# Kernel tuning notes

Hardware: AMD Instinct MI355X
Metric: run time of the kernel (lower is better)

The kernel has to match this reference:

```python
import jax, jax.numpy as jnp
import numpy as np

T, N, H = 512, 256, 256
HR, WC = 64, 128   # mdp rows (== n_actions), mdp cols
V = 64             # size of 'values' observation


def setup_inputs() -> dict:
    key = jax.random.key(0)
    ks = jax.random.split(key, 20)
    def p(i, shape):
        return (jax.random.normal(ks[i], shape, jnp.float32) / np.sqrt(shape[0])).astype(jnp.float32)
    z = lambda *s: jnp.zeros(s, jnp.float32)
    return dict(
        values=jax.random.normal(ks[0], (T, N, V), jnp.float32),
        mdp=jax.random.normal(ks[1], (N, HR, WC), jnp.float32),
        actions=jax.random.randint(ks[2], (T, N), 0, HR),
        a0=jax.random.randint(ks[3], (N,), 0, HR),
        h0=jax.random.normal(ks[4], (N, H), jnp.float32) * 0.1,
        emb_W=p(5, (WC, H)), emb_b=z(H),
        gfw_Wih=p(6, (H, 3 * H)), gfw_Whh=p(7, (H, 3 * H)), gfw_bih=z(3 * H), gfw_bhh=z(3 * H),
        gbw_Wih=p(8, (H, 3 * H)), gbw_Whh=p(9, (H, 3 * H)), gbw_bih=z(3 * H), gbw_bhh=z(3 * H),
        f0_W=p(10, (V + H, H)), f0_b=z(H),
        f1_W=p(11, (H, H)), f1_b=z(H),
        cell_Wih=p(12, (H, 3 * H)), cell_Whh=p(13, (H, 3 * H)), cell_bih=z(3 * H), cell_bhh=z(3 * H),
        critic_W=p(14, (H, 1)), critic_b=z(1),
        qg_W=p(15, (H, 2 * H)), qg_b=z(2 * H),
    )


def gru_step(x, h, Wih, Whh, bih, bhh):
    # torch GRU gate math: gates ordered (reset, update, new)
    gi = x @ Wih + bih
    gh = h @ Whh + bhh
    ir, iz, in_ = jnp.split(gi, 3, axis=-1)
    hr, hz, hn = jnp.split(gh, 3, axis=-1)
    r = jax.nn.sigmoid(ir + hr)
    z = jax.nn.sigmoid(iz + hz)
    n = jnp.tanh(in_ + r * hn)
    return (1.0 - z) * n + z * h


def run_gru(seq, Wih, Whh, bih, bhh):
    # seq: (S, N, H) -> outputs (S, N, H), zero initial state (torch default)
    h0g = jnp.zeros((seq.shape[1], Whh.shape[0]), seq.dtype)
    def step(h, x):
        hn = gru_step(x, h, Wih, Whh, bih, bhh)
        return hn, hn
    _, out = jax.lax.scan(step, h0g, seq)
    return out


def _forward(values, mdp, actions, a0, h0,
             emb_W, emb_b,
             gfw_Wih, gfw_Whh, gfw_bih, gfw_bhh,
             gbw_Wih, gbw_Whh, gbw_bih, gbw_bhh,
             f0_W, f0_b, f1_W, f1_b,
             cell_Wih, cell_Whh, cell_bih, cell_bhh,
             critic_W, critic_b, qg_W, qg_b):
    M = mdp @ emb_W + emb_b                      # (N, HR, H) line embeddings
    seq = jnp.swapaxes(M, 0, 1)                  # (HR, N, H) seq-first
    Kf = run_gru(seq, gfw_Wih, gfw_Whh, gfw_bih, gfw_bhh)
    Kb = run_gru(seq[::-1], gbw_Wih, gbw_Whh, gbw_bih, gbw_bhh)[::-1]
    K = jnp.swapaxes(jnp.concatenate([Kf, Kb], -1), 0, 1)   # (N, HR, 2H)

    a_prev = jnp.concatenate([a0[None], actions[:-1]], axis=0)  # A[t-1], t=0 wraps to hx.a
    batch = jnp.arange(M.shape[0])

    def step(h, xs):
        v_t, ap, ac = xs
        r = M[batch, ap]                         # one-hot(a_prev) @ M == row gather, (N, H)
        x = jnp.concatenate([v_t, r], axis=-1)
        x = jax.nn.relu(x @ f0_W + f0_b)
        x = jax.nn.relu(x @ f1_W + f1_b)
        h = gru_step(x, h, cell_Wih, cell_Whh, cell_bih, cell_bhh)
        k = h @ qg_W + qg_b                      # (N, 2H) query
        logits = jnp.einsum('nsd,nd->ns', K, k)  # (N, HR)
        probs = jax.nn.softmax(logits, axis=-1)
        v = h @ critic_W + critic_b              # (N, 1)
        return h, (ac.astype(jnp.float32)[:, None], v, h, probs)

    _, (a_out, v_out, h_out, p_out) = jax.lax.scan(step, h0, (values, a_prev, actions))
    # pack() order: RecurrentState fields 'a v h a_probs'
    hx = jnp.concatenate([a_out, v_out, h_out, p_out], axis=-1)  # (T, N, 2+H+HR)
    return hx


def reference(values, mdp, actions, a0, h0,
              emb_W, emb_b,
              gfw_Wih, gfw_Whh, gfw_bih, gfw_bhh,
              gbw_Wih, gbw_Whh, gbw_bih, gbw_bhh,
              f0_W, f0_b, f1_W, f1_b,
              cell_Wih, cell_Whh, cell_bih, cell_bhh,
              critic_W, critic_b, qg_W, qg_b):
    return _forward(values, mdp, actions, a0, h0,
                    emb_W, emb_b,
                    gfw_Wih, gfw_Whh, gfw_bih, gfw_bhh,
                    gbw_Wih, gbw_Whh, gbw_bih, gbw_bhh,
                    f0_W, f0_b, f1_W, f1_b,
                    cell_Wih, cell_Whh, cell_bih, cell_bhh,
                    critic_W, critic_b, qg_W, qg_b)
```

## Files before the change

kernel.cpp:

```cpp
#include <hip/hip_runtime.h>

#define TSTEPS 512
#define NBATCH 256
#define HID    256
#define TCHUNK 64
#define NCHUNK 8

typedef __attribute__((ext_vector_type(8))) short bf16x8;
typedef __attribute__((ext_vector_type(4))) float f32x4;

__device__ __forceinline__ unsigned short f2b(float x) {
    union { float f; unsigned int u; } c; c.f = x;
    unsigned int u = c.u;
    return (unsigned short)((u + 0x7fffu + ((u >> 16) & 1u)) >> 16);
}

__device__ __forceinline__ void gload_lds16(const float* g, float* l) {
    __builtin_amdgcn_global_load_lds(
        (const __attribute__((address_space(1))) unsigned int*)g,
        (__attribute__((address_space(3))) unsigned int*)l,
        16, 0, 0);
}

__device__ __forceinline__ int swzi(int row, int g) {
// ... 76 lines not shown
                C[(long)row * ldc + col] = v;
            }
        }
}

__global__ void combine_bias(const float* a0, const float* b0,
                             const float* a1, const float* b1,
                             const float* a2, const float* b2,
                             float* o0, float* o1, float* o2)
{
    int i = blockIdx.x * 256 + threadIdx.x;
    o0[i] = a0[i] + b0[i];
    o1[i] = a1[i] + b1[i];
    o2[i] = a2[i] + b2[i];
}

__global__ void seq_major(const float* __restrict__ M, float* __restrict__ Mseq)
{
    int b = blockIdx.x;
    int s = b >> 8, n = b & 255;
    int t = threadIdx.x;
    Mseq[(long)b * 256 + t] = M[((long)n * 64 + s) * 256 + t];
}

__global__ __launch_bounds__(256) void pack_w(
    const float* __restrict__ Wf, const float* __restrict__ Wb, const float* __restrict__ Wc,
    unsigned short* __restrict__ Pf, unsigned short* __restrict__ Pb, unsigned short* __restrict__ Pc)
{
    int chunk = blockIdx.x * 256 + threadIdx.x;
    const float* W = (blockIdx.y == 0) ? Wf : ((blockIdx.y == 1) ? Wb : Wc);
    unsigned short* P = (blockIdx.y == 0) ? Pf : ((blockIdx.y == 1) ? Pb : Pc);
    int lane = chunk & 63;
    int kt   = (chunk >> 6) & 7;
    int f    = (chunk >> 9) % 6;
    int w    = chunk / 3072;
    int g = f >> 1, hh = f & 1;
    int c = lane & 15, q = lane >> 4;
    int col = g * 256 + w * 32 + hh * 16 + c;
    int k0  = kt * 32 + q * 8;
    unsigned int v[8];
#pragma unroll
    for (int j = 0; j < 8; j++) v[j] = f2b(W[(long)(k0 + j) * 768 + col]);
    uint4 o;
    o.x = v[0] | (v[1] << 16); o.y = v[2] | (v[3] << 16);
    o.z = v[4] | (v[5] << 16); o.w = v[6] | (v[7] << 16);
    *(uint4*)&P[(long)chunk * 8] = o;
}

__global__ void build_x(const float* __restrict__ values, const float* __restrict__ Mbuf,
                        const int* __restrict__ actions, const int* __restrict__ a0,
                        float* __restrict__ Xc, int t0)
{
    int m = blockIdx.x;
    int tl = m >> 8, n = m & 255;
    int t = t0 + tl;
    int c = threadIdx.x;
    float v;
    if (c < 64) {
        v = values[((long)t * 256 + n) * 64 + c];
    } else {
        int ap = (t == 0) ? a0[n] : actions[(long)(t - 1) * 256 + n];
        v = Mbuf[((long)n * 64 + ap) * 256 + (c - 64)];
    }
    Xc[(long)m * 320 + c] = v;
}

struct GemmRole {
    const float* A; const float* B; const float* bias; float* C;
    int K; long lda; long ldb; long ldc; int act; int nblocks; int ntn;
};

union FusedLds {
    struct { unsigned short hbuf[2][16][264]; float gibuf[2][16 * 772]; } s;
    struct { unsigned short As[64][32]; unsigned short Bs[128][32]; } g;
    struct { unsigned short As2[2][64][32]; unsigned short Bs2[2][64][32]; } l;
};

__device__ __forceinline__ void scan_role(FusedLds* L,
    const float* gi, const unsigned short* PK, const float* h_init,
    float* outp, float* h_state, int n0, int steps, int kgru, int d)
{
    auto& hbuf  = L->s.hbuf;
    auto& gibuf = L->s.gibuf;
    const int tid = threadIdx.x;
    const int w = tid >> 6, lane = tid & 63;
    const int q = lane >> 4, c = lane & 15, q8 = q << 3;
    const int wcol = w * 32;

    bf16x8 Bf[6][8];
#pragma unroll
    for (int f = 0; f < 6; f++)
#pragma unroll
        for (int kt = 0; kt < 8; kt++)
            Bf[f][kt] = *(const bf16x8*)&PK[(((long)(w * 6 + f) * 8 + kt) * 64 + lane) * 8];

    f32x4 hreg[2];
#pragma unroll
    for (int hh = 0; hh < 2; hh++)
#pragma unroll
        for (int rg = 0; rg < 4; rg++) {
            float v = 0.f;
            if (!kgru) v = h_init[(long)(n0 + q * 4 + rg) * 256 + wcol + hh * 16 + c];
            hreg[hh][rg] = v;
            hbuf[1][q * 4 + rg][wcol + hh * 16 + c] = f2b(v);
        }

    const int row0 = kgru ? (d ? 63 : 0) : 0;
    const long gstride = (kgru && d) ? -196608L : 196608L;
    const float* gsrc = gi + ((long)row0 * 256 + n0) * 768;
    float* optr[4];
    long ostride;
    if (kgru) {
        ostride = d ? -512L : 512L;
#pragma unroll
        for (int rg = 0; rg < 4; rg++)
            optr[rg] = outp + ((long)(n0 + q * 4 + rg) * 64 + row0) * 512 + d * 256 + wcol + c;
    } else {
        ostride = 65536L;
#pragma unroll
        for (int rg = 0; rg < 4; rg++)
            optr[rg] = outp + (long)(n0 + q * 4 + rg) * 256 + wcol + c;
    }

#pragma unroll
    for (int i = 0; i < 6; i++) {
        int idx = w * 6 + i;
        int r = idx / 3, ch = idx % 3;
        gload_lds16(gsrc + (long)r * 768 + ch * 256 + lane * 4,
                    &gibuf[0][r * 772 + ch * 256]);
    }
    __syncthreads();

    for (int s = 0; s < steps; s++) {
        const int cur = s & 1;
        if (s + 1 < steps) {
            const float* src = gsrc + gstride;
#pragma unroll
            for (int i = 0; i < 6; i++) {
                int idx = w * 6 + i;
                int r = idx / 3, ch = idx % 3;
                gload_lds16(src + (long)r * 768 + ch * 256 + lane * 4,
                            &gibuf[cur ^ 1][r * 772 + ch * 256]);
            }
        }
        gsrc += gstride;
        asm volatile("" ::: "memory");

        const unsigned short* hrd = &hbuf[cur ^ 1][0][0];
        const float* gp = &gibuf[cur][(q * 4) * 772 + wcol + c];
        unsigned short* hwr = &hbuf[cur][q * 4][wcol + c];

#pragma unroll
        for (int hh = 0; hh < 2; hh++) {
            f32x4 ar = (f32x4){0.f, 0.f, 0.f, 0.f};
            f32x4 az = (f32x4){0.f, 0.f, 0.f, 0.f};
            f32x4 an = (f32x4){0.f, 0.f, 0.f, 0.f};
#pragma unroll
            for (int kt = 0; kt < 8; kt++) {
                bf16x8 a = *(const bf16x8*)&hrd[c * 264 + kt * 32 + q8];
                ar = __builtin_amdgcn_mfma_f32_16x16x32_bf16(a, Bf[0 + hh][kt], ar, 0, 0, 0);
                az = __builtin_amdgcn_mfma_f32_16x16x32_bf16(a, Bf[2 + hh][kt], az, 0, 0, 0);
                an = __builtin_amdgcn_mfma_f32_16x16x32_bf16(a, Bf[4 + hh][kt], an, 0, 0, 0);
            }
#pragma unroll
            for (int rg = 0; rg < 4; rg++) {
                float gr = gp[rg * 772 +       hh * 16];
                float gz = gp[rg * 772 + 256 + hh * 16];
                float gn = gp[rg * 772 + 512 + hh * 16];
                float r  = __builtin_amdgcn_rcpf(1.f + __expf(-(gr + ar[rg])));
                float zg = __builtin_amdgcn_rcpf(1.f + __expf(-(gz + az[rg])));
                float nn = 1.f - 2.f * __builtin_amdgcn_rcpf(1.f + __expf(2.f * (gn + r * an[rg])));
                float hv = (1.f - zg) * nn + zg * hreg[hh][rg];
                hreg[hh][rg] = hv;
                hwr[rg * 264 + hh * 16] = f2b(hv);
                optr[rg][hh * 16] = hv;
            }
            asm volatile("" ::: "memory");
        }

#pragma unroll
        for (int rg = 0; rg < 4; rg++) optr[rg] += ostride;

        asm volatile("s_waitcnt vmcnt(8) lgkmcnt(0)" ::: "memory");
        __builtin_amdgcn_sched_barrier(0);
        __builtin_amdgcn_s_barrier();
        __builtin_amdgcn_sched_barrier(0);
    }

    if (!kgru) {
#pragma unroll
        for (int hh = 0; hh < 2; hh++)
#pragma unroll
            for (int rg = 0; rg < 4; rg++)
                h_state[(long)(n0 + q * 4 + rg) * 256 + wcol + hh * 16 + c] = hreg[hh][rg];
    }
}

__device__ __forceinline__ void gemm_role(FusedLds* L, const GemmRole& R, int rb)
{
    auto& As = L->g.As;
    auto& Bs = L->g.Bs;
    const int tid = threadIdx.x;
    const int lane = tid & 63, w = tid >> 6;
    const int mt = rb / R.ntn, nt = rb % R.ntn;
    const long m0 = (long)mt * 64, n0 = (long)nt * 128;
    const int wr = (w >> 2) * 32, wc = (w & 3) * 32;

    f32x4 acc[2][2];
#pragma unroll
    for (int i = 0; i < 2; i++)
#pragma unroll
        for (int j = 0; j < 2; j++) acc[i][j] = (f32x4){0.f, 0.f, 0.f, 0.f};

    for (int k0 = 0; k0 < R.K; k0 += 32) {
        {
            const int r = tid >> 3, ck = (tid & 7) << 2;
            const float* s = R.A + (m0 + r) * R.lda + k0 + ck;
            float4 v = *(const float4*)s;
            unsigned short* dp = &As[r][swzi(r, ck >> 3) + (ck & 7)];
            dp[0] = f2b(v.x); dp[1] = f2b(v.y); dp[2] = f2b(v.z); dp[3] = f2b(v.w);
        }
        {
            const int kk = tid >> 4, cn = (tid & 15) << 3;
            const float* s = R.B + (long)(k0 + kk) * R.ldb + n0 + cn;
            float4 v0 = *(const float4*)s, v1 = *(const float4*)(s + 4);
            const int sc = swzi(cn, kk >> 3) + (kk & 7);
            Bs[cn + 0][sc] = f2b(v0.x); Bs[cn + 1][sc] = f2b(v0.y);
            Bs[cn + 2][sc] = f2b(v0.z); Bs[cn + 3][sc] = f2b(v0.w);
            Bs[cn + 4][sc] = f2b(v1.x); Bs[cn + 5][sc] = f2b(v1.y);
            Bs[cn + 6][sc] = f2b(v1.z); Bs[cn + 7][sc] = f2b(v1.w);
        }
        __syncthreads();
        const int l15 = lane & 15, q = lane >> 4;
        bf16x8 a0 = *(const bf16x8*)&As[wr +      l15][swzi(wr +      l15, q)];
        bf16x8 a1 = *(const bf16x8*)&As[wr + 16 + l15][swzi(wr + 16 + l15, q)];
        bf16x8 b0 = *(const bf16x8*)&Bs[wc +      l15][swzi(wc +      l15, q)];
        bf16x8 b1 = *(const bf16x8*)&Bs[wc + 16 + l15][swzi(wc + 16 + l15, q)];
        acc[0][0] = __builtin_amdgcn_mfma_f32_16x16x32_bf16(a0, b0, acc[0][0], 0, 0, 0);
        acc[0][1] = __builtin_amdgcn_mfma_f32_16x16x32_bf16(a0, b1, acc[0][1], 0, 0, 0);
        acc[1][0] = __builtin_amdgcn_mfma_f32_16x16x32_bf16(a1, b0, acc[1][0], 0, 0, 0);
        acc[1][1] = __builtin_amdgcn_mfma_f32_16x16x32_bf16(a1, b1, acc[1][1], 0, 0, 0);
        __syncthreads();
    }
    const int cq = lane >> 4, cc = lane & 15;
#pragma unroll
    for (int i = 0; i < 2; i++)
#pragma unroll
        for (int j = 0; j < 2; j++) {
#pragma unroll
            for (int rg = 0; rg < 4; rg++) {
                long row = m0 + wr + i * 16 + cq * 4 + rg;
                long col = n0 + wc + j * 16 + cc;
                float v = acc[i][j][rg];
                if (R.bias) v += R.bias[col];
                if (R.act == 1) v = v > 0.f ? v : 0.f;
                R.C[row * R.ldc + col] = v;
            }
        }
}

__device__ __forceinline__ void logits_role(FusedLds* L, int rb,
    const float* Qs, const float* Kb, float* Lout)
{
    auto& As = L->l.As2;
    auto& Bs = L->l.Bs2;
    const int tid = threadIdx.x;
    const int half = tid >> 8, htid = tid & 255;
    const int z = rb * 2 + half;
    const float* A = Qs + (long)z * 512;
    const float* B = Kb + (long)z * 32768;
    float* C = Lout + (long)z * 64;
    const int lane = htid & 63, w4 = htid >> 6;
    const int wr = (w4 >> 1) * 32, wc = (w4 & 1) * 32;

    f32x4 acc[2][2];
#pragma unroll
    for (int i = 0; i < 2; i++)
#pragma unroll
        for (int j = 0; j < 2; j++) acc[i][j] = (f32x4){0.f, 0.f, 0.f, 0.f};

    for (int k0 = 0; k0 < 512; k0 += 32) {
        const int r = htid >> 2, ck = (htid & 3) << 3;
        {
            const float* s = A + (long)r * 131072 + k0 + ck;
            float4 v0 = *(const float4*)s, v1 = *(const float4*)(s + 4);
            unsigned short* d = &As[half][r][swzi(r, ck >> 3)];
            d[0] = f2b(v0.x); d[1] = f2b(v0.y); d[2] = f2b(v0.z); d[3] = f2b(v0.w);
            d[4] = f2b(v1.x); d[5] = f2b(v1.y); d[6] = f2b(v1.z); d[7] = f2b(v1.w);
        }
        {
            const float* s = B + (long)r * 512 + k0 + ck;
            float4 v0 = *(const float4*)s, v1 = *(const float4*)(s + 4);
            unsigned short* d = &Bs[half][r][swzi(r, ck >> 3)];
            d[0] = f2b(v0.x); d[1] = f2b(v0.y); d[2] = f2b(v0.z); d[3] = f2b(v0.w);
            d[4] = f2b(v1.x); d[5] = f2b(v1.y); d[6] = f2b(v1.z); d[7] = f2b(v1.w);
        }
        __syncthreads();
        const int l15 = lane & 15, q = lane >> 4;
        bf16x8 a0 = *(const bf16x8*)&As[half][wr +      l15][swzi(wr +      l15, q)];
        bf16x8 a1 = *(const bf16x8*)&As[half][wr + 16 + l15][swzi(wr + 16 + l15, q)];
        bf16x8 b0 = *(const bf16x8*)&Bs[half][wc +      l15][swzi(wc +      l15, q)];
        bf16x8 b1 = *(const bf16x8*)&Bs[half][wc + 16 + l15][swzi(wc + 16 + l15, q)];
        acc[0][0] = __builtin_amdgcn_mfma_f32_16x16x32_bf16(a0, b0, acc[0][0], 0, 0, 0);
        acc[0][1] = __builtin_amdgcn_mfma_f32_16x16x32_bf16(a0, b1, acc[0][1], 0, 0, 0);
        acc[1][0] = __builtin_amdgcn_mfma_f32_16x16x32_bf16(a1, b0, acc[1][0], 0, 0, 0);
        acc[1][1] = __builtin_amdgcn_mfma_f32_16x16x32_bf16(a1, b1, acc[1][1], 0, 0, 0);
        __syncthreads();
    }
    const int cq = lane >> 4, cc = lane & 15;
#pragma unroll
    for (int i = 0; i < 2; i++)
#pragma unroll
        for (int j = 0; j < 2; j++) {
#pragma unroll
            for (int rg = 0; rg < 4; rg++)
                C[(long)(wr + i * 16 + cq * 4 + rg) * 16384 + wc + j * 16 + cc] = acc[i][j][rg];
        }
}

__device__ __forceinline__ void epi_role(int rb,
    const float* Hall, const float* Lc, const int* actions,
    const float* critic_W, const float* critic_b, float* out, int t0)
{
    const int w = threadIdx.x >> 6, j = threadIdx.x & 63;
    const int m = rb * 8 + w;
    const int tl = m >> 8, n = m & 255;
    const int t = t0 + tl;
    long o = ((long)t * 256 + n) * 322;
    const float* h = Hall + (long)m * 256;
    float part = 0.f;
#pragma unroll
    for (int i = 0; i < 4; i++) {
        float hv = h[j + 64 * i];
        out[o + 2 + j + 64 * i] = hv;
        part += hv * critic_W[j + 64 * i];
    }
    for (int off = 32; off > 0; off >>= 1) part += __shfl_down(part, off);
    if (j == 0) {
        out[o]     = (float)actions[(long)t * 256 + n];
        out[o + 1] = part + critic_b[0];
    }
    float x = Lc[(long)m * 64 + j];
    float mx = x;
    for (int off = 32; off > 0; off >>= 1) mx = fmaxf(mx, __shfl_down(mx, off));
    mx = __shfl(mx, 0);
    float e = __expf(x - mx);
    float ssum = e;
    for (int off = 32; off > 0; off >>= 1) ssum += __shfl_down(ssum, off);
    ssum = __shfl(ssum, 0);
    out[o + 258 + j] = e / ssum;
}

__device__ __forceinline__ void bx_role(int rb,
    const float* values, const float* Mbuf, const int* actions, const int* a0,
    float* Xd, int t0)
{
    const int tid = threadIdx.x;
    if (tid >= 320) return;
    for (int rr = 0; rr < 128; rr++) {
        int m = rb * 128 + rr;
        int tl = m >> 8, n = m & 255;
        int t = t0 + tl;
        float v;
        if (tid < 64) {
            v = values[((long)t * 256 + n) * 64 + tid];
        } else {
            int ap = (t == 0) ? a0[n] : actions[(long)(t - 1) * 256 + n];
            v = Mbuf[((long)n * 64 + ap) * 256 + (tid - 64)];
        }
        Xd[(long)m * 320 + tid] = v;
    }
}

__global__ __launch_bounds__(512, 2) void fused_k(
    const float* sc_gi, const unsigned short* sc_PK, const float* sc_hinit,
    float* sc_out, float* sc_hstate,
    int kgru_nblk, const float* kg_gi0, const float* kg_gi1,
    const unsigned short* kg_PK0, const unsigned short* kg_PK1, float* kg_out,
    GemmRole g0, GemmRole g1, GemmRole g2, GemmRole g3,
    int lg_nblk, const float* lg_Q, const float* lg_K, float* lg_L,
    int ep_nblk, const float* ep_Hall, const float* ep_L, int ep_t0,
    int bx_nblk, const float* values, const float* Mbuf,
    const int* actions, const int* a0, float* bx_dst, int bx_t0,
    const float* critic_W, const float* critic_b, float* out)
{
    __shared__ __align__(16) FusedLds L;
    int b = blockIdx.x;
    if (b < 16) {
        scan_role(&L, sc_gi, sc_PK, sc_hinit, sc_out, sc_hstate, b * 16, TCHUNK, 0, 0);
        return;
    }
    b -= 16;
    if (b < kgru_nblk) {
        int d = b >> 4, n0 = (b & 15) * 16;
        scan_role(&L, d ? kg_gi1 : kg_gi0, d ? kg_PK1 : kg_PK0, nullptr,
                  kg_out, nullptr, n0, 64, 1, d);
        return;
    }
    b -= kgru_nblk;
    if (b < g0.nblocks) { gemm_role(&L, g0, b); return; }
    b -= g0.nblocks;
    if (b < g1.nblocks) { gemm_role(&L, g1, b); return; }
    b -= g1.nblocks;
    if (b < g2.nblocks) { gemm_role(&L, g2, b); return; }
    b -= g2.nblocks;
    if (b < g3.nblocks) { gemm_role(&L, g3, b); return; }
    b -= g3.nblocks;
    if (b < lg_nblk) { logits_role(&L, b, lg_Q, lg_K, lg_L); return; }
    b -= lg_nblk;
    if (b < ep_nblk) { epi_role(b, ep_Hall, ep_L, actions, critic_W, critic_b, out, ep_t0); return; }
    b -= ep_nblk;
    if (b < bx_nblk) bx_role(b, values, Mbuf, actions, a0, bx_dst, bx_t0);
}

__global__ __launch_bounds__(64) void epilogue_k(
    const float* __restrict__ Hallc, const float* __restrict__ Lc,
    const int* __restrict__ actions,
    const float* __restrict__ critic_W, const float* __restrict__ critic_b,
    float* __restrict__ out, int t0)
{
    int m = blockIdx.x;
    int tl = m >> 8, n = m & 255;
    int t = t0 + tl;
    int j = threadIdx.x;
    long o = ((long)t * 256 + n) * 322;
    const float* h = Hallc + (long)m * 256;
    float part = 0.f;
#pragma unroll
    for (int i = 0; i < 4; i++) {
        float hv = h[j + 64 * i];
        out[o + 2 + j + 64 * i] = hv;
        part += hv * critic_W[j + 64 * i];
    }
    for (int off = 32; off > 0; off >>= 1) part += __shfl_down(part, off);
    if (j == 0) {
        out[o]     = (float)actions[(long)t * 256 + n];
        out[o + 1] = part + critic_b[0];
    }
    float x = Lc[(long)m * 64 + j];
    float mx = x;
    for (int off = 32; off > 0; off >>= 1) mx = fmaxf(mx, __shfl_down(mx, off));
    mx = __shfl(mx, 0);
    float e = __expf(x - mx);
    float ssum = e;
    for (int off = 32; off > 0; off >>= 1) ssum += __shfl_down(ssum, off);
// ... 27 lines not shown
    const float* cell_Wih = (const float*)d_in[19];
    const float* cell_Whh = (const float*)d_in[20];
    const float* cell_bih = (const float*)d_in[21];
    const float* cell_bhh = (const float*)d_in[22];
    const float* critic_W = (const float*)d_in[23];
    const float* critic_b = (const float*)d_in[24];
    const float* qg_W     = (const float*)d_in[25];
    const float* qg_b     = (const float*)d_in[26];
    float* out = (float*)d_out;

    char* base = (char*)d_ws;
    size_t off = 0;
    auto alloc = [&](size_t nf) -> float* {
        float* p = (float*)(base + off);
        off += nf * sizeof(float);
        off = (off + 255) & ~(size_t)255;
        return p;
    };
    float* Mbuf   = alloc(16384ull * 256);
    float* Mseq   = alloc(16384ull * 256);
    float* gfA    = alloc(16384ull * 768);
    float* gbA    = alloc(16384ull * 768);
    float* Kbuf   = alloc(256ull * 64 * 512);
    float* PKf    = alloc(98304);
    float* PKb    = alloc(98304);
    float* PKc    = alloc(98304);
    float* hstate = alloc(256ull * 256);
    float* Xr[2]    = { alloc(16384ull * 320), alloc(16384ull * 320) };
    float* X0r[2]   = { alloc(16384ull * 256), alloc(16384ull * 256) };
    float* X1r[2]   = { alloc(16384ull * 256), alloc(16384ull * 256) };
    float* GIr[2]   = { alloc(16384ull * 768), alloc(16384ull * 768) };
    float* Hallr[4] = { alloc(16384ull * 256), alloc(16384ull * 256),
                        Mseq, alloc(16384ull * 256) };
    float* Qr[2]  = { gfA, gbA };
    float* Lr[2]  = { alloc(16384ull * 64), alloc(16384ull * 64) };
    float* bias_f = alloc(768);
    float* bias_b = alloc(768);
    float* bias_c = alloc(768);
    (void)ws_size; (void)in_sizes; (void)n_in; (void)out_size;

    dim3 blk(256);

    gemm_f32<false, 0><<<dim3(4, 256, 1), blk, 0, stream>>>(
        mdp, 128, 0, emb_W, 256, 0, emb_b, Mbuf, 256, 0, 16384, 256, 128);
    seq_major<<<dim3(16384), blk, 0, stream>>>(Mbuf, Mseq);
    pack_w<<<dim3(96, 3, 1), blk, 0, stream>>>(
        gfw_Whh, gbw_Whh, cell_Whh,
        (unsigned short*)PKf, (unsigned short*)PKb, (unsigned short*)PKc);
    combine_bias<<<dim3(3), blk, 0, stream>>>(gfw_bih, gfw_bhh, gbw_bih, gbw_bhh,
                                              cell_bih, cell_bhh, bias_f, bias_b, bias_c);
    gemm_f32<false, 0><<<dim3(12, 256, 1), blk, 0, stream>>>(
        Mseq, 256, 0, gfw_Wih, 768, 0, bias_f, gfA, 768, 0, 16384, 768, 256);
    gemm_f32<false, 0><<<dim3(12, 256, 1), blk, 0, stream>>>(
        Mseq, 256, 0, gbw_Wih, 768, 0, bias_b, gbA, 768, 0, 16384, 768, 256);

    build_x<<<dim3(16384), dim3(320), 0, stream>>>(values, Mbuf, actions, a0, Xr[0], 0);
    gemm_f32<false, 1><<<dim3(4, 256, 1), blk, 0, stream>>>(
        Xr[0], 320, 0, f0_W, 256, 0, f0_b, X0r[0], 256, 0, 16384, 256, 320);
    build_x<<<dim3(16384), dim3(320), 0, stream>>>(values, Mbuf, actions, a0, Xr[1], 64);
    gemm_f32<false, 1><<<dim3(4, 256, 1), blk, 0, stream>>>(
        Xr[1], 320, 0, f0_W, 256, 0, f0_b, X0r[1], 256, 0, 16384, 256, 320);
    gemm_f32<false, 1><<<dim3(4, 256, 1), blk, 0, stream>>>(
        X0r[0], 256, 0, f1_W, 256, 0, f1_b, X1r[0], 256, 0, 16384, 256, 256);
    build_x<<<dim3(16384), dim3(320), 0, stream>>>(values, Mbuf, actions, a0, Xr[0], 128);
    gemm_f32<false, 1><<<dim3(4, 256, 1), blk, 0, stream>>>(
        Xr[0], 320, 0, f0_W, 256, 0, f0_b, X0r[0], 256, 0, 16384, 256, 320);
    gemm_f32<false, 1><<<dim3(4, 256, 1), blk, 0, stream>>>(
        X0r[1], 256, 0, f1_W, 256, 0, f1_b, X1r[1], 256, 0, 16384, 256, 256);
    build_x<<<dim3(16384), dim3(320), 0, stream>>>(values, Mbuf, actions, a0, Xr[1], 192);
    gemm_f32<false, 0><<<dim3(12, 256, 1), blk, 0, stream>>>(
        X1r[0], 256, 0, cell_Wih, 768, 0, bias_c, GIr[0], 768, 0, 16384, 768, 256);

    for (int c = 0; c < NCHUNK; c++) {
        GemmRole g0{}, g1{}, g2{}, g3{};
        if (c <= 4) g0 = GemmRole{ Xr[(c + 1) & 1], f0_W, f0_b, X0r[(c + 1) & 1],
                                   320, 320, 256, 256, 1, 512, 2 };
        if (c <= 5) g1 = GemmRole{ X0r[c & 1], f1_W, f1_b, X1r[c & 1],
                                   256, 256, 256, 256, 1, 512, 2 };
        if (c <= 6) g2 = GemmRole{ X1r[(c + 1) & 1], cell_Wih, bias_c, GIr[(c + 1) & 1],
                                   256, 256, 768, 768, 0, 1536, 6 };
        if (c >= 1) g3 = GemmRole{ Hallr[(c - 1) & 3], qg_W, qg_b, Qr[(c - 1) & 1],
                                   256, 256, 512, 512, 0, 1024, 4 };
        int kgn = (c == 0) ? 32 : 0;
        int lgn = (c >= 2) ? 128 : 0;
        int epn = (c >= 3) ? 2048 : 0;
        int bxn = (c <= 3) ? 128 : 0;
        int total = 16 + kgn + g0.nblocks + g1.nblocks + g2.nblocks + g3.nblocks
                    + lgn + epn + bxn;

        fused_k<<<dim3(total), dim3(512), 0, stream>>>(
            GIr[c & 1], (const unsigned short*)PKc, (c == 0) ? h0 : (const float*)hstate,
            Hallr[c & 3], hstate,
            kgn, gfA, gbA, (const unsigned short*)PKf, (const unsigned short*)PKb, Kbuf,
            g0, g1, g2, g3,
            lgn, Qr[(c - 2) & 1], Kbuf, Lr[(c - 2) & 1],
            epn, Hallr[(c - 3) & 3], Lr[(c - 3) & 1], (c - 3) * 64,
            bxn, values, Mbuf, actions, a0, Xr[c & 1], (c + 4) * 64,
            critic_W, critic_b, out);
    }

    epilogue_k<<<dim3(16384), dim3(64), 0, stream>>>(
        Hallr[1], Lr[1], actions, critic_W, critic_b, out, 5 * 64);
    gemm_f32<false, 0><<<dim3(8, 256, 1), blk, 0, stream>>>(
        Hallr[3], 256, 0, qg_W, 512, 0, qg_b, Qr[1], 512, 0, 16384, 512, 256);
    gemm_f32<true, 0><<<dim3(1, 1, 256), blk, 0, stream>>>(
        Qr[0], 131072, 512, Kbuf, 512, 32768, nullptr, Lr[0], 16384, 64, 64, 64, 512);
    epilogue_k<<<dim3(16384), dim3(64), 0, stream>>>(
        Hallr[2], Lr[0], actions, critic_W, critic_b, out, 6 * 64);
    gemm_f32<true, 0><<<dim3(1, 1, 256), blk, 0, stream>>>(
        Qr[1], 131072, 512, Kbuf, 512, 32768, nullptr, Lr[1], 16384, 64, 64, 64, 512);
    epilogue_k<<<dim3(16384), dim3(64), 0, stream>>>(
        Hallr[3], Lr[1], actions, critic_W, critic_b, out, 7 * 64);
}
```

Before: 2.123 ms.

## Halve fused kernel block size to 256 threads with 4 waves per scan block

The fused persistent kernel moves from 512 to 256 threads per block. Each scan wave now owns 64 hidden columns with 12 B fragments held in registers, and the packed weight layout changes to match. The MFMA passes for the four column groups are interleaved with the gate math so tensor work overlaps the transcendental math, and the h tile is loaded into registers once per step. GEMM and logits roles are retiled to 64x64 tiles with twice as many blocks, and the build_x role is adjusted for 256 threads. The aim is cheaper barriers per sequential step on the latency-bound recurrence, at the cost of much higher register pressure (96 bf16x8 weight fragments per lane) and possible spilling.

Result: slower. 4.819 ms (+127.0%).

```diff
diff --git a/kernel.cpp b/kernel.cpp
--- a/kernel.cpp
+++ b/kernel.cpp
@@ -132,11 +132,11 @@
     unsigned short* P = (blockIdx.y == 0) ? Pf : ((blockIdx.y == 1) ? Pb : Pc);
     int lane = chunk & 63;
     int kt   = (chunk >> 6) & 7;
-    int f    = (chunk >> 9) % 6;
-    int w    = chunk / 3072;
-    int g = f >> 1, hh = f & 1;
+    int f    = (chunk >> 9) % 12;
+    int w    = chunk / 6144;
+    int g = f >> 2, hh = f & 3;
     int c = lane & 15, q = lane >> 4;
-    int col = g * 256 + w * 32 + hh * 16 + c;
+    int col = g * 256 + w * 64 + hh * 16 + c;
     int k0  = kt * 32 + q * 8;
     unsigned int v[8];
 #pragma unroll
@@ -172,9 +172,38 @@
 
 union FusedLds {
     struct { unsigned short hbuf[2][16][264]; float gibuf[2][16 * 772]; } s;
-    struct { unsigned short As[64][32]; unsigned short Bs[128][32]; } g;
-    struct { unsigned short As2[2][64][32]; unsigned short Bs2[2][64][32]; } l;
+    struct { unsigned short As[64][32]; unsigned short Bs[64][32]; } g;
 };
+
+#define MPASS(HH, PR, PZ, PN)                                                  \
+    do {                                                                       \
+        PR = (f32x4){0.f, 0.f, 0.f, 0.f};                                      \
+        PZ = (f32x4){0.f, 0.f, 0.f, 0.f};                                      \
+        PN = (f32x4){0.f, 0.f, 0.f, 0.f};                                      \
+        _Pragma("unroll")                                                      \
+        for (int kt = 0; kt < 8; kt++) {                                       \
+            PR = __builtin_amdgcn_mfma_f32_16x16x32_bf16(a[kt], Bf[0 + HH][kt], PR, 0, 0, 0); \
+            PZ = __builtin_amdgcn_mfma_f32_16x16x32_bf16(a[kt], Bf[4 + HH][kt], PZ, 0, 0, 0); \
+            PN = __builtin_amdgcn_mfma_f32_16x16x32_bf16(a[kt], Bf[8 + HH][kt], PN, 0, 0, 0); \
+        }                                                                      \
+    } while (0)
+
+#define GATES(HH, PR, PZ, PN)                                                  \
+    do {                                                                       \
+        _Pragma("unroll")                                                      \
+        for (int rg = 0; rg < 4; rg++) {                                       \
+            float gr = gp[rg * 772 +       HH * 16];                           \
+            float gz = gp[rg * 772 + 256 + HH * 16];                           \
+            float gn = gp[rg * 772 + 512 + HH * 16];                           \
+            float r  = __builtin_amdgcn_rcpf(1.f + __expf(-(gr + PR[rg])));    \
+            float zg = __builtin_amdgcn_rcpf(1.f + __expf(-(gz + PZ[rg])));    \
+            float nn = 1.f - 2.f * __builtin_amdgcn_rcpf(1.f + __expf(2.f * (gn + r * PN[rg]))); \
+            float hv = (1.f - zg) * nn + zg * hreg[HH][rg];                    \
+            hreg[HH][rg] = hv;                                                 \
+            hwr[rg * 264 + HH * 16] = f2b(hv);                                 \
+            optr[rg][HH * 16] = hv;                                            \
+        }                                                                      \
+    } while (0)
 
 __device__ __forceinline__ void scan_role(FusedLds* L,
     const float* gi, const unsigned short* PK, const float* h_init,
@@ -185,18 +214,18 @@
     const int tid = threadIdx.x;
     const int w = tid >> 6, lane = tid & 63;
     const int q = lane >> 4, c = lane & 15, q8 = q << 3;
-    const int wcol = w * 32;
-
-    bf16x8 Bf[6][8];
-#pragma unroll
-    for (int f = 0; f < 6; f++)
+    const int wcol = w * 64;
+
+    bf16x8 Bf[12][8];
+#pragma unroll
+    for (int f = 0; f < 12; f++)
 #pragma unroll
         for (int kt = 0; kt < 8; kt++)
-            Bf[f][kt] = *(const bf16x8*)&PK[(((long)(w * 6 + f) * 8 + kt) * 64 + lane) * 8];
-
-    f32x4 hreg[2];
-#pragma unroll
-    for (int hh = 0; hh < 2; hh++)
+            Bf[f][kt] = *(const bf16x8*)&PK[(((long)(w * 12 + f) * 8 + kt) * 64 + lane) * 8];
+
+    f32x4 hreg[4];
+#pragma unroll
+    for (int hh = 0; hh < 4; hh++)
 #pragma unroll
         for (int rg = 0; rg < 4; rg++) {
             float v = 0.f;
@@ -223,8 +252,8 @@
     }
 
 #pragma unroll
-    for (int i = 0; i < 6; i++) {
-        int idx = w * 6 + i;
+    for (int i = 0; i < 12; i++) {
+        int idx = w * 12 + i;
         int r = idx / 3, ch = idx % 3;
         gload_lds16(gsrc + (long)r * 768 + ch * 256 + lane * 4,
                     &gibuf[0][r * 772 + ch * 256]);
@@ -233,11 +262,12 @@
 
     for (int s = 0; s < steps; s++) {
         const int cur = s & 1;
+
         if (s + 1 < steps) {
             const float* src = gsrc + gstride;
 #pragma unroll
-            for (int i = 0; i < 6; i++) {
-                int idx = w * 6 + i;
+            for (int i = 0; i < 12; i++) {
+                int idx = w * 12 + i;
                 int r = idx / 3, ch = idx % 3;
                 gload_lds16(src + (long)r * 768 + ch * 256 + lane * 4,
                             &gibuf[cur ^ 1][r * 772 + ch * 256]);
@@ -250,38 +280,25 @@
         const float* gp = &gibuf[cur][(q * 4) * 772 + wcol + c];
         unsigned short* hwr = &hbuf[cur][q * 4][wcol + c];
 
-#pragma unroll
-        for (int hh = 0; hh < 2; hh++) {
-            f32x4 ar = (f32x4){0.f, 0.f, 0.f, 0.f};
-            f32x4 az = (f32x4){0.f, 0.f, 0.f, 0.f};
-            f32x4 an = (f32x4){0.f, 0.f, 0.f, 0.f};
-#pragma unroll
-            for (int kt = 0; kt < 8; kt++) {
-                bf16x8 a = *(const bf16x8*)&hrd[c * 264 + kt * 32 + q8];
-                ar = __builtin_amdgcn_mfma_f32_16x16x32_bf16(a, Bf[0 + hh][kt], ar, 0, 0, 0);
-                az = __builtin_amdgcn_mfma_f32_16x16x32_bf16(a, Bf[2 + hh][kt], az, 0, 0, 0);
-                an = __builtin_amdgcn_mfma_f32_16x16x32_bf16(a, Bf[4 + hh][kt], an, 0, 0, 0);
-            }
-#pragma unroll
-            for (int rg = 0; rg < 4; rg++) {
-                float gr = gp[rg * 772 +       hh * 16];
-                float gz = gp[rg * 772 + 256 + hh * 16];
-                float gn = gp[rg * 772 + 512 + hh * 16];
-                float r  = __builtin_amdgcn_rcpf(1.f + __expf(-(gr + ar[rg])));
-                float zg = __builtin_amdgcn_rcpf(1.f + __expf(-(gz + az[rg])));
-                float nn = 1.f - 2.f * __builtin_amdgcn_rcpf(1.f + __expf(2.f * (gn + r * an[rg])));
-                float hv = (1.f - zg) * nn + zg * hreg[hh][rg];
-                hreg[hh][rg] = hv;
-                hwr[rg * 264 + hh * 16] = f2b(hv);
-                optr[rg][hh * 16] = hv;
-            }
-            asm volatile("" ::: "memory");
-        }
+        bf16x8 a[8];
+#pragma unroll
+        for (int kt = 0; kt < 8; kt++)
+            a[kt] = *(const bf16x8*)&hrd[c * 264 + kt * 32 + q8];
+
+        f32x4 p0r, p0z, p0n, p1r, p1z, p1n;
+        MPASS(0, p0r, p0z, p0n);
+        MPASS(1, p1r, p1z, p1n);
+        GATES(0, p0r, p0z, p0n);
+        MPASS(2, p0r, p0z, p0n);
+        GATES(1, p1r, p1z, p1n);
+        MPASS(3, p1r, p1z, p1n);
+        GATES(2, p0r, p0z, p0n);
+        GATES(3, p1r, p1z, p1n);
 
 #pragma unroll
         for (int rg = 0; rg < 4; rg++) optr[rg] += ostride;
 
-        asm volatile("s_waitcnt vmcnt(8) lgkmcnt(0)" ::: "memory");
+        asm volatile("s_waitcnt vmcnt(16) lgkmcnt(0)" ::: "memory");
         __builtin_amdgcn_sched_barrier(0);
         __builtin_amdgcn_s_barrier();
         __builtin_amdgcn_sched_barrier(0);
@@ -289,7 +306,7 @@
 
     if (!kgru) {
 #pragma unroll
-        for (int hh = 0; hh < 2; hh++)
+        for (int hh = 0; hh < 4; hh++)
 #pragma unroll
             for (int rg = 0; rg < 4; rg++)
                 h_state[(long)(n0 + q * 4 + rg) * 256 + wcol + hh * 16 + c] = hreg[hh][rg];
@@ -303,8 +320,8 @@
     const int tid = threadIdx.x;
     const int lane = tid & 63, w = tid >> 6;
     const int mt = rb / R.ntn, nt = rb % R.ntn;
-    const long m0 = (long)mt * 64, n0 = (long)nt * 128;
-    const int wr = (w >> 2) * 32, wc = (w & 3) * 32;
+    const long m0 = (long)mt * 64, n0 = (long)nt * 64;
+    const int wr = (w >> 1) * 32, wc = (w & 1) * 32;
 
     f32x4 acc[2][2];
 #pragma unroll
@@ -314,14 +331,15 @@
 
     for (int k0 = 0; k0 < R.K; k0 += 32) {
         {
-            const int r = tid >> 3, ck = (tid & 7) << 2;
+            const int r = tid >> 2, ck = (tid & 3) << 3;
             const float* s = R.A + (m0 + r) * R.lda + k0 + ck;
-            float4 v = *(const float4*)s;
-            unsigned short* dp = &As[r][swzi(r, ck >> 3) + (ck & 7)];
-            dp[0] = f2b(v.x); dp[1] = f2b(v.y); dp[2] = f2b(v.z); dp[3] = f2b(v.w);
+            float4 v0 = *(const float4*)s, v1 = *(const float4*)(s + 4);
+            unsigned short* d = &As[r][swzi(r, ck >> 3)];
+            d[0] = f2b(v0.x); d[1] = f2b(v0.y); d[2] = f2b(v0.z); d[3] = f2b(v0.w);
+            d[4] = f2b(v1.x); d[5] = f2b(v1.y); d[6] = f2b(v1.z); d[7] = f2b(v1.w);
         }
         {
-            const int kk = tid >> 4, cn = (tid & 15) << 3;
+            const int kk = tid >> 3, cn = (tid & 7) << 3;
             const float* s = R.B + (long)(k0 + kk) * R.ldb + n0 + cn;
             float4 v0 = *(const float4*)s, v1 = *(const float4*)(s + 4);
             const int sc = swzi(cn, kk >> 3) + (kk & 7);
@@ -362,16 +380,15 @@
 __device__ __forceinline__ void logits_role(FusedLds* L, int rb,
     const float* Qs, const float* Kb, float* Lout)
 {
-    auto& As = L->l.As2;
-    auto& Bs = L->l.Bs2;
+    auto& As = L->g.As;
+    auto& Bs = L->g.Bs;
     const int tid = threadIdx.x;
-    const int half = tid >> 8, htid = tid & 255;
-    const int z = rb * 2 + half;
+    const int z = rb;
     const float* A = Qs + (long)z * 512;
     const float* B = Kb + (long)z * 32768;
     float* C = Lout + (long)z * 64;
-    const int lane = htid & 63, w4 = htid >> 6;
-    const int wr = (w4 >> 1) * 32, wc = (w4 & 1) * 32;
+    const int lane = tid & 63, w = tid >> 6;
+    const int wr = (w >> 1) * 32, wc = (w & 1) * 32;
 
     f32x4 acc[2][2];
 #pragma unroll
@@ -380,27 +397,27 @@
         for (int j = 0; j < 2; j++) acc[i][j] = (f32x4){0.f, 0.f, 0.f, 0.f};
 
     for (int k0 = 0; k0 < 512; k0 += 32) {
-        const int r = htid >> 2, ck = (htid & 3) << 3;
+        const int r = tid >> 2, ck = (tid & 3) << 3;
         {
             const float* s = A + (long)r * 131072 + k0 + ck;
             float4 v0 = *(const float4*)s, v1 = *(const float4*)(s + 4);
-            unsigned short* d = &As[half][r][swzi(r, ck >> 3)];
+            unsigned short* d = &As[r][swzi(r, ck >> 3)];
             d[0] = f2b(v0.x); d[1] = f2b(v0.y); d[2] = f2b(v0.z); d[3] = f2b(v0.w);
             d[4] = f2b(v1.x); d[5] = f2b(v1.y); d[6] = f2b(v1.z); d[7] = f2b(v1.w);
         }
         {
             const float* s = B + (long)r * 512 + k0 + ck;
             float4 v0 = *(const float4*)s, v1 = *(const float4*)(s + 4);
-            unsigned short* d = &Bs[half][r][swzi(r, ck >> 3)];
+            unsigned short* d = &Bs[r][swzi(r, ck >> 3)];
             d[0] = f2b(v0.x); d[1] = f2b(v0.y); d[2] = f2b(v0.z); d[3] = f2b(v0.w);
             d[4] = f2b(v1.x); d[5] = f2b(v1.y); d[6] = f2b(v1.z); d[7] = f2b(v1.w);
         }
         __syncthreads();
         const int l15 = lane & 15, q = lane >> 4;
-        bf16x8 a0 = *(const bf16x8*)&As[half][wr +      l15][swzi(wr +      l15, q)];
-        bf16x8 a1 = *(const bf16x8*)&As[half][wr + 16 + l15][swzi(wr + 16 + l15, q)];
-        bf16x8 b0 = *(const bf16x8*)&Bs[half][wc +      l15][swzi(wc +      l15, q)];
-        bf16x8 b1 = *(const bf16x8*)&Bs[half][wc + 16 + l15][swzi(wc + 16 + l15, q)];
+        bf16x8 a0 = *(const bf16x8*)&As[wr +      l15][swzi(wr +      l15, q)];
+        bf16x8 a1 = *(const bf16x8*)&As[wr + 16 + l15][swzi(wr + 16 + l15, q)];
+        bf16x8 b0 = *(const bf16x8*)&Bs[wc +      l15][swzi(wc +      l15, q)];
+        bf16x8 b1 = *(const bf16x8*)&Bs[wc + 16 + l15][swzi(wc + 16 + l15, q)];
         acc[0][0] = __builtin_amdgcn_mfma_f32_16x16x32_bf16(a0, b0, acc[0][0], 0, 0, 0);
         acc[0][1] = __builtin_amdgcn_mfma_f32_16x16x32_bf16(a0, b1, acc[0][1], 0, 0, 0);
         acc[1][0] = __builtin_amdgcn_mfma_f32_16x16x32_bf16(a1, b0, acc[1][0], 0, 0, 0);
@@ -423,7 +440,7 @@
     const float* critic_W, const float* critic_b, float* out, int t0)
 {
     const int w = threadIdx.x >> 6, j = threadIdx.x & 63;
-    const int m = rb * 8 + w;
+    const int m = rb * 4 + w;
     const int tl = m >> 8, n = m & 255;
     const int t = t0 + tl;
     long o = ((long)t * 256 + n) * 322;
@@ -456,23 +473,21 @@
     float* Xd, int t0)
 {
     const int tid = threadIdx.x;
-    if (tid >= 320) return;
     for (int rr = 0; rr < 128; rr++) {
         int m = rb * 128 + rr;
         int tl = m >> 8, n = m & 255;
         int t = t0 + tl;
+        int ap = (t == 0) ? a0[n] : actions[(long)(t - 1) * 256 + n];
         float v;
-        if (tid < 64) {
-            v = values[((long)t * 256 + n) * 64 + tid];
-        } else {
-            int ap = (t == 0) ? a0[n] : actions[(long)(t - 1) * 256 + n];
-            v = Mbuf[((long)n * 64 + ap) * 256 + (tid - 64)];
-        }
+        if (tid < 64) v = values[((long)t * 256 + n) * 64 + tid];
+        else          v = Mbuf[((long)n * 64 + ap) * 256 + (tid - 64)];
         Xd[(long)m * 320 + tid] = v;
-    }
-}
-
-__global__ __launch_bounds__(512, 2) void fused_k(
+        if (tid < 64)
+            Xd[(long)m * 320 + 256 + tid] = Mbuf[((long)n * 64 + ap) * 256 + 192 + tid];
+    }
+}
+
+__global__ __launch_bounds__(256, 1) void fused_k(
     const float* sc_gi, const unsigned short* sc_PK, const float* sc_hinit,
     float* sc_out, float* sc_hstate,
     int kgru_nblk, const float* kg_gi0, const float* kg_gi1,
@@ -646,21 +661,21 @@
     for (int c = 0; c < NCHUNK; c++) {
         GemmRole g0{}, g1{}, g2{}, g3{};
         if (c <= 4) g0 = GemmRole{ Xr[(c + 1) & 1], f0_W, f0_b, X0r[(c + 1) & 1],
-                                   320, 320, 256, 256, 1, 512, 2 };
+                                   320, 320, 256, 256, 1, 1024, 4 };
         if (c <= 5) g1 = GemmRole{ X0r[c & 1], f1_W, f1_b, X1r[c & 1],
-                                   256, 256, 256, 256, 1, 512, 2 };
+                                   256, 256, 256, 256, 1, 1024, 4 };
         if (c <= 6) g2 = GemmRole{ X1r[(c + 1) & 1], cell_Wih, bias_c, GIr[(c + 1) & 1],
-                                   256, 256, 768, 768, 0, 1536, 6 };
+                                   256, 256, 768, 768, 0, 3072, 12 };
         if (c >= 1) g3 = GemmRole{ Hallr[(c - 1) & 3], qg_W, qg_b, Qr[(c - 1) & 1],
-                                   256, 256, 512, 512, 0, 1024, 4 };
+                                   256, 256, 512, 512, 0, 2048, 8 };
         int kgn = (c == 0) ? 32 : 0;
-        int lgn = (c >= 2) ? 128 : 0;
-        int epn = (c >= 3) ? 2048 : 0;
+        int lgn = (c >= 2) ? 256 : 0;
+        int epn = (c >= 3) ? 4096 : 0;
         int bxn = (c <= 3) ? 128 : 0;
         int total = 16 + kgn + g0.nblocks + g1.nblocks + g2.nblocks + g3.nblocks
                     + lgn + epn + bxn;
 
-        fused_k<<<dim3(total), dim3(512), 0, stream>>>(
+        fused_k<<<dim3(total), dim3(256), 0, stream>>>(
             GIr[c & 1], (const unsigned short*)PKc, (c == 0) ? h0 : (const float*)hstate,
             Hallr[c & 3], hstate,
             kgn, gfA, gbA, (const unsigned short*)PKf, (const unsigned short*)PKb, Kbuf,
```

## Fold bidirectional GRU input GEMMs and tail kernels into fused chunk launches

Applied to the files above, without the earlier changes.

Moves the two large forward/backward GRU input-projection GEMMs out of standalone launches into the first fused chunk kernel as extra gemm roles, and delays the key-GRU scan to chunk 1 so it consumes their results. The tail epilogue, query GEMM and logits launches are merged into two fused_k launches so these independent stages run concurrently. Qr[0] gets its own buffer because gfA is now written during chunk 0 while still needed later. This cuts launch count and serialization, at the cost of making chunk 0 heavier and relying on ordering across launches for the gfA/gbA dependency.

Result: slower. 2.202 ms (+3.7%).

```diff
diff --git a/kernel.cpp b/kernel.cpp
--- a/kernel.cpp
+++ b/kernel.cpp
@@ -473,11 +473,11 @@
 }
 
 __global__ __launch_bounds__(512, 2) void fused_k(
-    const float* sc_gi, const unsigned short* sc_PK, const float* sc_hinit,
+    int sc_nblk, const float* sc_gi, const unsigned short* sc_PK, const float* sc_hinit,
     float* sc_out, float* sc_hstate,
     int kgru_nblk, const float* kg_gi0, const float* kg_gi1,
     const unsigned short* kg_PK0, const unsigned short* kg_PK1, float* kg_out,
-    GemmRole g0, GemmRole g1, GemmRole g2, GemmRole g3,
+    GemmRole g0, GemmRole g1, GemmRole g2, GemmRole g3, GemmRole g4, GemmRole g5,
     int lg_nblk, const float* lg_Q, const float* lg_K, float* lg_L,
     int ep_nblk, const float* ep_Hall, const float* ep_L, int ep_t0,
     int bx_nblk, const float* values, const float* Mbuf,
@@ -486,11 +486,11 @@
 {
     __shared__ __align__(16) FusedLds L;
     int b = blockIdx.x;
-    if (b < 16) {
+    if (b < sc_nblk) {
         scan_role(&L, sc_gi, sc_PK, sc_hinit, sc_out, sc_hstate, b * 16, TCHUNK, 0, 0);
         return;
     }
-    b -= 16;
+    b -= sc_nblk;
     if (b < kgru_nblk) {
         int d = b >> 4, n0 = (b & 15) * 16;
         scan_role(&L, d ? kg_gi1 : kg_gi0, d ? kg_PK1 : kg_PK0, nullptr,
@@ -506,6 +506,10 @@
     b -= g2.nblocks;
     if (b < g3.nblocks) { gemm_role(&L, g3, b); return; }
     b -= g3.nblocks;
+    if (b < g4.nblocks) { gemm_role(&L, g4, b); return; }
+    b -= g4.nblocks;
+    if (b < g5.nblocks) { gemm_role(&L, g5, b); return; }
+    b -= g5.nblocks;
     if (b < lg_nblk) { logits_role(&L, b, lg_Q, lg_K, lg_L); return; }
     b -= lg_nblk;
     if (b < ep_nblk) { epi_role(b, ep_Hall, ep_L, actions, critic_W, critic_b, out, ep_t0); return; }
@@ -604,7 +608,7 @@
     float* GIr[2]   = { alloc(16384ull * 768), alloc(16384ull * 768) };
     float* Hallr[4] = { alloc(16384ull * 256), alloc(16384ull * 256),
                         Mseq, alloc(16384ull * 256) };
-    float* Qr[2]  = { gfA, gbA };
+    float* Qr[2]  = { alloc(16384ull * 512), gbA };
     float* Lr[2]  = { alloc(16384ull * 64), alloc(16384ull * 64) };
     float* bias_f = alloc(768);
     float* bias_b = alloc(768);
@@ -621,10 +625,6 @@
         (unsigned short*)PKf, (unsigned short*)PKb, (unsigned short*)PKc);
     combine_bias<<<dim3(3), blk, 0, stream>>>(gfw_bih, gfw_bhh, gbw_bih, gbw_bhh,
                                               cell_bih, cell_bhh, bias_f, bias_b, bias_c);
-    gemm_f32<false, 0><<<dim3(12, 256, 1), blk, 0, stream>>>(
-        Mseq, 256, 0, gfw_Wih, 768, 0, bias_f, gfA, 768, 0, 16384, 768, 256);
-    gemm_f32<false, 0><<<dim3(12, 256, 1), blk, 0, stream>>>(
-        Mseq, 256, 0, gbw_Wih, 768, 0, bias_b, gbA, 768, 0, 16384, 768, 256);
 
     build_x<<<dim3(16384), dim3(320), 0, stream>>>(values, Mbuf, actions, a0, Xr[0], 0);
     gemm_f32<false, 1><<<dim3(4, 256, 1), blk, 0, stream>>>(
@@ -644,7 +644,7 @@
         X1r[0], 256, 0, cell_Wih, 768, 0, bias_c, GIr[0], 768, 0, 16384, 768, 256);
 
     for (int c = 0; c < NCHUNK; c++) {
-        GemmRole g0{}, g1{}, g2{}, g3{};
+        GemmRole g0{}, g1{}, g2{}, g3{}, g4{}, g5{};
         if (c <= 4) g0 = GemmRole{ Xr[(c + 1) & 1], f0_W, f0_b, X0r[(c + 1) & 1],
                                    320, 320, 256, 256, 1, 512, 2 };
         if (c <= 5) g1 = GemmRole{ X0r[c & 1], f1_W, f1_b, X1r[c & 1],
@@ -653,34 +653,51 @@
                                    256, 256, 768, 768, 0, 1536, 6 };
         if (c >= 1) g3 = GemmRole{ Hallr[(c - 1) & 3], qg_W, qg_b, Qr[(c - 1) & 1],
                                    256, 256, 512, 512, 0, 1024, 4 };
-        int kgn = (c == 0) ? 32 : 0;
+        if (c == 0) {
+            g4 = GemmRole{ Mseq, gfw_Wih, bias_f, gfA, 256, 256, 768, 768, 0, 1536, 6 };
+            g5 = GemmRole{ Mseq, gbw_Wih, bias_b, gbA, 256, 256, 768, 768, 0, 1536, 6 };
+        }
+        int kgn = (c == 1) ? 32 : 0;
         int lgn = (c >= 2) ? 128 : 0;
         int epn = (c >= 3) ? 2048 : 0;
         int bxn = (c <= 3) ? 128 : 0;
         int total = 16 + kgn + g0.nblocks + g1.nblocks + g2.nblocks + g3.nblocks
-                    + lgn + epn + bxn;
+                    + g4.nblocks + g5.nblocks + lgn + epn + bxn;
 
         fused_k<<<dim3(total), dim3(512), 0, stream>>>(
-            GIr[c & 1], (const unsigned short*)PKc, (c == 0) ? h0 : (const float*)hstate,
+            16, GIr[c & 1], (const unsigned short*)PKc, (c == 0) ? h0 : (const float*)hstate,
             Hallr[c & 3], hstate,
             kgn, gfA, gbA, (const unsigned short*)PKf, (const unsigned short*)PKb, Kbuf,
-            g0, g1, g2, g3,
+            g0, g1, g2, g3, g4, g5,
             lgn, Qr[(c - 2) & 1], Kbuf, Lr[(c - 2) & 1],
             epn, Hallr[(c - 3) & 3], Lr[(c - 3) & 1], (c - 3) * 64,
             bxn, values, Mbuf, actions, a0, Xr[c & 1], (c + 4) * 64,
             critic_W, critic_b, out);
     }
 
-    epilogue_k<<<dim3(16384), dim3(64), 0, stream>>>(
-        Hallr[1], Lr[1], actions, critic_W, critic_b, out, 5 * 64);
-    gemm_f32<false, 0><<<dim3(8, 256, 1), blk, 0, stream>>>(
-        Hallr[3], 256, 0, qg_W, 512, 0, qg_b, Qr[1], 512, 0, 16384, 512, 256);
-    gemm_f32<true, 0><<<dim3(1, 1, 256), blk, 0, stream>>>(
-        Qr[0], 131072, 512, Kbuf, 512, 32768, nullptr, Lr[0], 16384, 64, 64, 64, 512);
-    epilogue_k<<<dim3(16384), dim3(64), 0, stream>>>(
-        Hallr[2], Lr[0], actions, critic_W, critic_b, out, 6 * 64);
-    gemm_f32<true, 0><<<dim3(1, 1, 256), blk, 0, stream>>>(
-        Qr[1], 131072, 512, Kbuf, 512, 32768, nullptr, Lr[1], 16384, 64, 64, 64, 512);
+    {
+        GemmRole gz{}, g3t = GemmRole{ Hallr[3], qg_W, qg_b, Qr[1],
+                                       256, 256, 512, 512, 0, 1024, 4 };
+        fused_k<<<dim3(1024 + 128 + 2048), dim3(512), 0, stream>>>(
+            0, GIr[0], (const unsigned short*)PKc, hstate, Hallr[0], hstate,
+            0, gfA, gbA, (const unsigned short*)PKf, (const unsigned short*)PKb, Kbuf,
+            gz, gz, gz, g3t, gz, gz,
+            128, Qr[0], Kbuf, Lr[0],
+            2048, Hallr[1], Lr[1], 5 * 64,
+            0, values, Mbuf, actions, a0, Xr[0], 0,
+            critic_W, critic_b, out);
+    }
+    {
+        GemmRole gz{};
+        fused_k<<<dim3(128 + 2048), dim3(512), 0, stream>>>(
+            0, GIr[0], (const unsigned short*)PKc, hstate, Hallr[0], hstate,
+            0, gfA, gbA, (const unsigned short*)PKf, (const unsigned short*)PKb, Kbuf,
+            gz, gz, gz, gz, gz, gz,
+            128, Qr[1], Kbuf, Lr[1],
+            2048, Hallr[2], Lr[0], 6 * 64,
+            0, values, Mbuf, actions, a0, Xr[0], 0,
+            critic_W, critic_b, out);
+    }
     epilogue_k<<<dim3(16384), dim3(64), 0, stream>>>(
         Hallr[3], Lr[1], actions, critic_W, critic_b, out, 7 * 64);
 }
```

## Fuse tail GEMM, logits and epilogue launches into combined tail kernels

Applied to the files above, without the earlier changes.

Replaces the sequence of separate tail launches (epilogue, Q GEMM, batched logits GEMM, epilogue, logits GEMM) with two launches of a new multi-role tail kernel. The new kernel uses a smaller LDS union and launch bounds that allow two blocks per CU. Independent work (Q projection, logits for the previous chunk, epilogue for an earlier chunk) can then run concurrently. Q for chunk 0 gets its own buffer instead of aliasing gfA, which avoids a hazard but costs extra memory.

New measurement: 2.096 ms. No clear change (-1.3%).

```diff
diff --git a/kernel.cpp b/kernel.cpp
--- a/kernel.cpp
+++ b/kernel.cpp
@@ -175,6 +175,10 @@
     struct { unsigned short As[64][32]; unsigned short Bs[128][32]; } g;
     struct { unsigned short As2[2][64][32]; unsigned short Bs2[2][64][32]; } l;
 };
+union TailLds {
+    struct { unsigned short As[64][32]; unsigned short Bs[128][32]; } g;
+    struct { unsigned short As2[2][64][32]; unsigned short Bs2[2][64][32]; } l;
+};
 
 __device__ __forceinline__ void scan_role(FusedLds* L,
     const float* gi, const unsigned short* PK, const float* h_init,
@@ -296,10 +300,9 @@
     }
 }
 
-__device__ __forceinline__ void gemm_role(FusedLds* L, const GemmRole& R, int rb)
-{
-    auto& As = L->g.As;
-    auto& Bs = L->g.Bs;
+__device__ __forceinline__ void gemm_role_impl(
+    unsigned short (*As)[32], unsigned short (*Bs)[32], const GemmRole& R, int rb)
+{
     const int tid = threadIdx.x;
     const int lane = tid & 63, w = tid >> 6;
     const int mt = rb / R.ntn, nt = rb % R.ntn;
@@ -359,11 +362,10 @@
         }
 }
 
-__device__ __forceinline__ void logits_role(FusedLds* L, int rb,
+__device__ __forceinline__ void logits_role_impl(
+    unsigned short (*As)[64][32], unsigned short (*Bs)[64][32], int rb,
     const float* Qs, const float* Kb, float* Lout)
 {
-    auto& As = L->l.As2;
-    auto& Bs = L->l.Bs2;
     const int tid = threadIdx.x;
     const int half = tid >> 8, htid = tid & 255;
     const int z = rb * 2 + half;
@@ -498,19 +500,34 @@
         return;
     }
     b -= kgru_nblk;
-    if (b < g0.nblocks) { gemm_role(&L, g0, b); return; }
+    if (b < g0.nblocks) { gemm_role_impl(L.g.As, L.g.Bs, g0, b); return; }
     b -= g0.nblocks;
-    if (b < g1.nblocks) { gemm_role(&L, g1, b); return; }
+    if (b < g1.nblocks) { gemm_role_impl(L.g.As, L.g.Bs, g1, b); return; }
     b -= g1.nblocks;
-    if (b < g2.nblocks) { gemm_role(&L, g2, b); return; }
+    if (b < g2.nblocks) { gemm_role_impl(L.g.As, L.g.Bs, g2, b); return; }
     b -= g2.nblocks;
-    if (b < g3.nblocks) { gemm_role(&L, g3, b); return; }
+    if (b < g3.nblocks) { gemm_role_impl(L.g.As, L.g.Bs, g3, b); return; }
     b -= g3.nblocks;
-    if (b < lg_nblk) { logits_role(&L, b, lg_Q, lg_K, lg_L); return; }
+    if (b < lg_nblk) { logits_role_impl(L.l.As2, L.l.Bs2, b, lg_Q, lg_K, lg_L); return; }
     b -= lg_nblk;
     if (b < ep_nblk) { epi_role(b, ep_Hall, ep_L, actions, critic_W, critic_b, out, ep_t0); return; }
     b -= ep_nblk;
     if (b < bx_nblk) bx_role(b, values, Mbuf, actions, a0, bx_dst, bx_t0);
+}
+
+__global__ __launch_bounds__(512, 2) void tail_k(
+    GemmRole g3,
+    int lg_nblk, const float* lg_Q, const float* lg_K, float* lg_L,
+    int ep_nblk, const float* ep_Hall, const float* ep_L, int ep_t0,
+    const int* actions, const float* critic_W, const float* critic_b, float* out)
+{
+    __shared__ __align__(16) TailLds L;
+    int b = blockIdx.x;
+    if (b < g3.nblocks) { gemm_role_impl(L.g.As, L.g.Bs, g3, b); return; }
+    b -= g3.nblocks;
+    if (b < lg_nblk) { logits_role_impl(L.l.As2, L.l.Bs2, b, lg_Q, lg_K, lg_L); return; }
+    b -= lg_nblk;
+    if (b < ep_nblk) epi_role(b, ep_Hall, ep_L, actions, critic_W, critic_b, out, ep_t0);
 }
 
 __global__ __launch_bounds__(64) void epilogue_k(
@@ -604,7 +621,7 @@
     float* GIr[2]   = { alloc(16384ull * 768), alloc(16384ull * 768) };
     float* Hallr[4] = { alloc(16384ull * 256), alloc(16384ull * 256),
                         Mseq, alloc(16384ull * 256) };
-    float* Qr[2]  = { gfA, gbA };
+    float* Qr[2]  = { alloc(16384ull * 512), gbA };
     float* Lr[2]  = { alloc(16384ull * 64), alloc(16384ull * 64) };
     float* bias_f = alloc(768);
     float* bias_b = alloc(768);
@@ -671,16 +688,21 @@
             critic_W, critic_b, out);
     }
 
-    epilogue_k<<<dim3(16384), dim3(64), 0, stream>>>(
-        Hallr[1], Lr[1], actions, critic_W, critic_b, out, 5 * 64);
-    gemm_f32<false, 0><<<dim3(8, 256, 1), blk, 0, stream>>>(
-        Hallr[3], 256, 0, qg_W, 512, 0, qg_b, Qr[1], 512, 0, 16384, 512, 256);
-    gemm_f32<true, 0><<<dim3(1, 1, 256), blk, 0, stream>>>(
-        Qr[0], 131072, 512, Kbuf, 512, 32768, nullptr, Lr[0], 16384, 64, 64, 64, 512);
-    epilogue_k<<<dim3(16384), dim3(64), 0, stream>>>(
-        Hallr[2], Lr[0], actions, critic_W, critic_b, out, 6 * 64);
-    gemm_f32<true, 0><<<dim3(1, 1, 256), blk, 0, stream>>>(
-        Qr[1], 131072, 512, Kbuf, 512, 32768, nullptr, Lr[1], 16384, 64, 64, 64, 512);
+    {
+        GemmRole g3t = GemmRole{ Hallr[3], qg_W, qg_b, Qr[1],
+                                 256, 256, 512, 512, 0, 1024, 4 };
+        tail_k<<<dim3(1024 + 128 + 2048), dim3(512), 0, stream>>>(
+            g3t, 128, Qr[0], Kbuf, Lr[0],
+            2048, Hallr[1], Lr[1], 5 * 64,
+            actions, critic_W, critic_b, out);
+    }
+    {
+        GemmRole gz{};
+        tail_k<<<dim3(128 + 2048), dim3(512), 0, stream>>>(
+            gz, 128, Qr[1], Kbuf, Lr[1],
+            2048, Hallr[2], Lr[0], 6 * 64,
+            actions, critic_W, critic_b, out);
+    }
     epilogue_k<<<dim3(16384), dim3(64), 0, stream>>>(
         Hallr[3], Lr[1], actions, critic_W, critic_b, out, 7 * 64);
 }
```
